# Performance work log

Hardware: AMD Instinct MI355X
Metric: run time of the kernel (lower is better)

The kernel has to match this reference:

```python
import jax, jax.numpy as jnp
import numpy as np

EPS = 1e-6  # clamp epsilon in GeM
NORM_EPS = 1e-12  # torch F.normalize eps
PATCH_SIZES = (3,)


def l2norm(x, axis):
    n = jnp.sqrt(jnp.sum(x * x, axis=axis, keepdims=True))
    return x / jnp.maximum(n, NORM_EPS)


def setup_inputs() -> dict:
    key = jax.random.key(0)
    k1, k2, k3 = jax.random.split(key, 3)
    N, D, H, W, F = 16, 2048, 32, 32, 512
    x = jax.random.normal(k1, (N, D, H, W), jnp.float32)
    proj_w = jax.random.normal(k2, (F, D), jnp.float32) * (1.0 / np.sqrt(D))
    proj_b = jax.random.normal(k3, (F,), jnp.float32) * 0.01
    p = jnp.full((1,), 3.0, jnp.float32)
    return {"x": x, "proj_w": proj_w, "proj_b": proj_b, "p": p}


def reference(x, proj_w, proj_b, p):
    # ---- GeM global descriptor (global_pool path inside local_pool) ----
    x = l2norm(x, axis=1)                                  # L2 over channel dim
    g = jnp.clip(x, EPS, None) ** p[0]                     # [N,D,H,W]
    g = g.mean(axis=(-2, -1))                              # [N,D]
    g = g ** (1.0 / p[0])
    g = g @ proj_w.T + proj_b                              # [N,F]
    g = l2norm(g, axis=1)

    # ---- integral image over spatial dims ----
    integ = jnp.cumsum(jnp.cumsum(x, axis=-1), axis=-2)    # [N,D,H,W]

    local_descs = []
    for ps in PATCH_SIZES:
        off = ps // 2
        # zero-pad (1+off) on top/left, then replicate-pad off on bottom/right
        ipad = jnp.pad(integ, ((0, 0), (0, 0), (1 + off, 0), (1 + off, 0)))
        ipad = jnp.pad(ipad, ((0, 0), (0, 0), (0, off), (0, off)), mode='edge')
        # box sum via 4-corner integral-image difference
        # == grouped 2x2 conv with dilation=ps, weights [[1,-1],[-1,1]], stride=1
        box = (ipad[:, :, :-ps, :-ps] - ipad[:, :, :-ps, ps:]
               - ipad[:, :, ps:, :-ps] + ipad[:, :, ps:, ps:])  # [N,D,H,W]
        N, D, Hh, Ww = box.shape
        pd = box.reshape(N, D, Hh * Ww).transpose(0, 2, 1)  # [N,HW,D]
        pd = pd @ proj_w.T + proj_b                         # [N,HW,F]
        pd = l2norm(pd, axis=2)
        local_descs.append(pd.transpose(0, 2, 1))           # [N,F,HW]

    return g, local_descs[0]
```

## Files before the change

### kernel.cpp

```cpp
#include <hip/hip_runtime.h>
#include <hip/hip_bf16.h>

#define N_ 16
#define D_ 2048
#define H_ 32
#define W_ 32
#define HW_ 1024
#define F_ 512

typedef unsigned short u16;
typedef unsigned int u32;
typedef __attribute__((ext_vector_type(8))) short bf16x8;
typedef __attribute__((ext_vector_type(4))) float f32x4;

__device__ __forceinline__ u16 f2bf(float f) {
  union { float fv; u32 u; } c; c.fv = f;
  u32 u = c.u;
  u32 r = (u + 0x7fffu + ((u >> 16) & 1u)) >> 16;
  return (u16)r;
}

#define GLD_LDS16(gp, lp) __builtin_amdgcn_global_load_lds( \
    (const __attribute__((address_space(1))) void*)(gp), \
    (__attribute__((address_space(3))) void*)(lp), 16, 0, 0)

__global__ __launch_bounds__(256) void k_zero(float* __restrict__ p) {
  int i = blockIdx.x * 256 + threadIdx.x;
  ((float4*)p)[i] = (float4){0.f, 0.f, 0.f, 0.f};
}

__global__ __launch_bounds__(256) void k_sumsq(const float* __restrict__ x, float* __restrict__ sumsq) {
  const int n = blockIdx.x;
  const int dc = blockIdx.y;
  const int t = threadIdx.x;
  const float* xp = x + ((size_t)n * D_ + (size_t)dc * 64) * HW_;
  float s0 = 0.f, s1 = 0.f, s2 = 0.f, s3 = 0.f;
  for (int d = 0; d < 64; ++d) {
    const float* row = xp + (size_t)d * HW_;
    float v0 = row[t], v1 = row[t + 256], v2 = row[t + 512], v3 = row[t + 768];
    s0 += v0 * v0; s1 += v1 * v1; s2 += v2 * v2; s3 += v3 * v3;
  }
  atomicAdd(&sumsq[n * HW_ + t      ], s0);
  atomicAdd(&sumsq[n * HW_ + t + 256], s1);
  atomicAdd(&sumsq[n * HW_ + t + 512], s2);
  atomicAdd(&sumsq[n * HW_ + t + 768], s3);
}

__global__ __launch_bounds__(256) void k_box2(const float* __restrict__ x,
    const float* __restrict__ sumsq, const float* __restrict__ pvec,
    float* __restrict__ gbuf, u16* __restrict__ packA) {
  const int n = blockIdx.x, ht = blockIdx.y, dc = blockIdx.z;
  const int h0 = ht * 4, d0 = dc * 64;
  const int t = threadIdx.x;
  const int w = t & 31, g = t >> 5;
  const float p = pvec[0];
  const bool p3 = (p == 3.0f);

  __shared__ __align__(16) u16 sbox[128 * 68];

  float rn[6];
  #pragma unroll
  for (int jj = 0; jj < 6; ++jj) {
    int hp = h0 - 1 + jj;
    float r = 0.f;
    if (hp >= 0 && hp < H_) r = 1.0f / fmaxf(sqrtf(sumsq[n * HW_ + hp * W_ + w]), 1e-12f);
    rn[jj] = r;
  }

  float s[8];
  #pragma unroll
  for (int j = 0; j < 8; ++j) s[j] = 0.f;

  #pragma unroll 2
  for (int j = 0; j < 8; ++j) {
    const int d = d0 + g * 8 + j;
    const float* col = x + ((size_t)(n * D_ + d)) * HW_ + w;
    float v[6];
    #pragma unroll
    for (int jj = 0; jj < 6; ++jj) {
      int hp = h0 - 1 + jj;
      float xv = (hp >= 0 && hp < H_) ? col[hp * W_] : 0.f;
      v[jj] = xv * rn[jj];
    }
    #pragma unroll
    for (int jj = 1; jj <= 4; ++jj) {
      float cv = fmaxf(v[jj], 1e-6f);
      s[j] += p3 ? cv * cv * cv : __powf(cv, p);
    }
    float hs[6];
    #pragma unroll
    for (int jj = 0; jj < 6; ++jj) {
      float l = __shfl_up(v[jj], 1, 32);
      float r = __shfl_down(v[jj], 1, 32);
      if (w == 0) l = 0.f;
      if (w == 31) r = 0.f;
      hs[jj] = l + v[jj] + r;
    }
    #pragma unroll
    for (int k = 0; k < 4; ++k) {
      float b = hs[k] + hs[k + 1] + hs[k + 2];
      sbox[(k * 32 + w) * 68 + g * 8 + j] = f2bf(b);
    }
  }
  __syncthreads();

  {
    const int r = t >> 1, half = t & 1;
    const u16* srcp = sbox + r * 68 + half * 32;
    uint2 a[8];
    #pragma unroll
    for (int q = 0; q < 8; ++q) a[q] = *(const uint2*)(srcp + q * 4);
    const int mt = n * 16 + ht * 2 + (r >> 6);
    const int mf = (r >> 4) & 3, r15 = r & 15;
    const int kt = dc * 2 + half;
    u16* dst = packA + ((size_t)(mt * 64 + kt) * 4 + mf) * 512 + r15 * 8;
    #pragma unroll
    for (int q = 0; q < 4; ++q) {
      uint4 b;
      b.x = a[2 * q].x; b.y = a[2 * q].y; b.z = a[2 * q + 1].x; b.w = a[2 * q + 1].y;
      *(uint4*)(dst + q * 128) = b;
    }
  }

  #pragma unroll
  for (int j = 0; j < 8; ++j) {
    float v = s[j];
    v += __shfl_xor(v, 16, 32);
    v += __shfl_xor(v, 8, 32);
    v += __shfl_xor(v, 4, 32);
    v += __shfl_xor(v, 2, 32);
    v += __shfl_xor(v, 1, 32);
    if (w == 0) atomicAdd(&gbuf[n * D_ + d0 + g * 8 + j], v);
  }
}

__global__ __launch_bounds__(256) void k_wconv(const float* __restrict__ w, u16* __restrict__ packB) {
  const int i = blockIdx.x * 256 + threadIdx.x;
  const int lane = i & 63, nf = (i >> 6) & 3, kt = (i >> 8) & 63, wq = i >> 14;
  const int r15 = lane & 15, hi = lane >> 4;
  const int f = wq * 64 + nf * 16 + r15;
  const int k = kt * 32 + hi * 8;
  const float* src = w + (size_t)f * D_ + k;
  float4 v0 = *(const float4*)(src);
  float4 v1 = *(const float4*)(src + 4);
  u16 r[8] = { f2bf(v0.x), f2bf(v0.y), f2bf(v0.z), f2bf(v0.w),
               f2bf(v1.x), f2bf(v1.y), f2bf(v1.z), f2bf(v1.w) };
  *(uint4*)(packB + (size_t)i * 8) = *(const uint4*)r;
}

__global__ __launch_bounds__(512) void k_gemm(const u16* __restrict__ packA,
    const u16* __restrict__ packB, const float* __restrict__ bias,
    float* __restrict__ outL) {
  const int n  = blockIdx.x >> 4;
  const int mtl = blockIdx.x & 15;
  const int mt = blockIdx.x;
  const int hw0 = mtl * 64;
  const int t = threadIdx.x;
  const int lane = t & 63, wv = t >> 6;
  const int r15 = lane & 15, hi = lane >> 4;

  __shared__ __align__(16) float smem_f[128 * 68];
  __shared__ float s_sq[8][64];
  __shared__ float s_rn[64];

  f32x4 acc[4][4];
  #pragma unroll
  for (int a = 0; a < 4; ++a)
    #pragma unroll
    for (int b = 0; b < 4; ++b) acc[a][b] = (f32x4){0.f, 0.f, 0.f, 0.f};

  const u16* asrc = packA + ((size_t)(mt * 64) * 4 + (wv & 3)) * 512 + lane * 8;
  const u16* bbase = packB + (size_t)wv * 131072 + lane * 8;

#define STAGE_A(KT) GLD_LDS16(asrc + (size_t)(KT) * 2048, \
    (char*)smem_f + ((KT) & 3) * 4096 + (wv & 3) * 1024)

  STAGE_A(0);
  STAGE_A(1);
  bf16x8 bc[4], bn[4];
  #pragma unroll
  for (int nf = 0; nf < 4; ++nf) bc[nf] = *(const bf16x8*)(bbase + nf * 512);

  for (int kt = 0; kt < 64; ++kt) {
    if (kt + 2 < 64) STAGE_A(kt + 2);
    if (kt + 1 < 64) {
      #pragma unroll
      for (int nf = 0; nf < 4; ++nf)
        bn[nf] = *(const bf16x8*)(bbase + ((kt + 1) * 4 + nf) * 512);
    }
    __builtin_amdgcn_sched_barrier(0);
    if (kt < 62) {
      asm volatile("s_waitcnt vmcnt(5)" ::: "memory");
    } else if (kt == 62) {
      asm volatile("s_waitcnt vmcnt(4)" ::: "memory");
    } else {
      asm volatile("s_waitcnt vmcnt(0)" ::: "memory");
    }
    __builtin_amdgcn_sched_barrier(0);
    __builtin_amdgcn_s_barrier();
    __builtin_amdgcn_sched_barrier(0);

    const u16* sA = (const u16*)((const char*)smem_f + (kt & 3) * 4096);
    bf16x8 af[4];
    #pragma unroll
    for (int mf = 0; mf < 4; ++mf)
      af[mf] = *(const bf16x8*)(sA + mf * 512 + lane * 8);
    #pragma unroll
    for (int mf = 0; mf < 4; ++mf)
      #pragma unroll
      for (int nf = 0; nf < 4; ++nf)
        acc[mf][nf] = __builtin_amdgcn_mfma_f32_16x16x32_bf16(af[mf], bc[nf], acc[mf][nf], 0, 0, 0);
    #pragma unroll
    for (int nf = 0; nf < 4; ++nf) bc[nf] = bn[nf];
  }
#undef STAGE_A

  float badd[4];
  #pragma unroll
  for (int nf = 0; nf < 4; ++nf) badd[nf] = bias[wv * 64 + nf * 16 + r15];
  #pragma unroll
  for (int mf = 0; mf < 4; ++mf)
    #pragma unroll
    for (int nf = 0; nf < 4; ++nf)
      #pragma unroll
      for (int j = 0; j < 4; ++j) acc[mf][nf][j] += badd[nf];

  #pragma unroll
  for (int mf = 0; mf < 4; ++mf)
    #pragma unroll
    for (int j = 0; j < 4; ++j) {
      float s = 0.f;
      #pragma unroll
      for (int nf = 0; nf < 4; ++nf) { float v = acc[mf][nf][j]; s += v * v; }
      s += __shfl_xor(s, 1); s += __shfl_xor(s, 2); s += __shfl_xor(s, 4); s += __shfl_xor(s, 8);
      if ((lane & 15) == 0) s_sq[wv][mf * 16 + hi * 4 + j] = s;
    }
  __syncthreads();
  if (t < 64) {
    float s = 0.f;
    #pragma unroll
    for (int w8 = 0; w8 < 8; ++w8) s += s_sq[w8][t];
    s_rn[t] = 1.0f / fmaxf(sqrtf(s), 1e-12f);
  }
  __syncthreads();

  float* ct = smem_f;
  for (int nf = 0; nf < 4; ++nf) {
    const int fi = wv * 16 + r15;
    #pragma unroll
    for (int mf = 0; mf < 4; ++mf)
      #pragma unroll
      for (int j = 0; j < 4; ++j) {
        int m = mf * 16 + hi * 4 + j;
        ct[fi * 68 + m] = acc[mf][nf][j] * s_rn[m];
      }
    __syncthreads();
    {
      int fr = t >> 2, mq = t & 3;
      int f = (fr >> 4) * 64 + nf * 16 + (fr & 15);
      float* dst = outL + ((size_t)(n * F_ + f)) * HW_ + hw0 + mq * 16;
      const float* srcp = ct + fr * 68 + mq * 16;
      float4 a0 = *(const float4*)(srcp);
      float4 a1 = *(const float4*)(srcp + 4);
      float4 a2 = *(const float4*)(srcp + 8);
      float4 a3 = *(const float4*)(srcp + 12);
      *(float4*)(dst) = a0; *(float4*)(dst + 4) = a1;
      *(float4*)(dst + 8) = a2; *(float4*)(dst + 12) = a3;
    }
    __syncthreads();
  }
}

__global__ __launch_bounds__(256) void k_gem_fin(const float* __restrict__ gbuf,
    const float* __restrict__ pvec, float* __restrict__ gg) {
  int i = blockIdx.x * 256 + threadIdx.x;
  float p = pvec[0];
  float m = gbuf[i] * (1.0f / 1024.0f);
  gg[i] = (p == 3.0f) ? cbrtf(m) : powf(m, 1.0f / p);
}

__global__ __launch_bounds__(256) void k_gproj(const float* __restrict__ w,
    const float* __restrict__ bias, const float* __restrict__ gg,
    float* __restrict__ gproj) {
  const int f = blockIdx.x;
  const int t = threadIdx.x;
  float wreg[8];
  #pragma unroll
  for (int j = 0; j < 8; ++j) wreg[j] = w[(size_t)f * D_ + t + j * 256];
  __shared__ float red[4];
  const int lane = t & 63, wv = t >> 6;
  for (int n = 0; n < N_; ++n) {
    float s = 0.f;
    #pragma unroll
    for (int j = 0; j < 8; ++j) s += wreg[j] * gg[n * D_ + t + j * 256];
    #pragma unroll
    for (int off = 32; off >= 1; off >>= 1) s += __shfl_down(s, off);
    if (lane == 0) red[wv] = s;
    __syncthreads();
    if (t == 0) gproj[n * F_ + f] = red[0] + red[1] + red[2] + red[3] + bias[f];
    __syncthreads();
  }
}

__global__ __launch_bounds__(512) void k_gnorm(const float* __restrict__ gproj, float* __restrict__ outg) {
  const int n = blockIdx.x;
  const int t = threadIdx.x;
  float v = gproj[n * F_ + t];
  float s = v * v;
  const int lane = t & 63, wv = t >> 6;
  #pragma unroll
  for (int off = 32; off >= 1; off >>= 1) s += __shfl_down(s, off);
  __shared__ float red[8];
  __shared__ float rtot;
  if (lane == 0) red[wv] = s;
  __syncthreads();
  if (t == 0) {
    float a = 0.f;
    #pragma unroll
    for (int i = 0; i < 8; ++i) a += red[i];
    rtot = 1.0f / fmaxf(sqrtf(a), 1e-12f);
  }
  __syncthreads();
  outg[n * F_ + t] = v * rtot;
}

extern "C" void kernel_launch(void* const* d_in, const int* in_sizes, int n_in,
                              void* d_out, int out_size, void* d_ws, size_t ws_size,
                              hipStream_t stream) {
  const float* x  = (const float*)d_in[0];
  const float* pw = (const float*)d_in[1];
  const float* pb = (const float*)d_in[2];
  const float* pv = (const float*)d_in[3];
  float* out = (float*)d_out;

  char* ws = (char*)d_ws;
  float* sumsq = (float*)ws;
  float* gbuf  = (float*)(ws + 65536);
  float* gg    = (float*)(ws + 65536 + 131072);
  float* gproj = (float*)(ws + 65536 + 2 * 131072);
  u16*   packB = (u16*)(ws + 65536 + 2 * 131072 + 32768);
  u16*   packA = (u16*)(ws + 4u * 1024u * 1024u);

  k_zero<<<dim3(48), dim3(256), 0, stream>>>(sumsq);
  k_sumsq<<<dim3(16, 32), dim3(256), 0, stream>>>(x, sumsq);
  k_wconv<<<dim3(512), dim3(256), 0, stream>>>(pw, packB);
  k_box2<<<dim3(16, 8, 32), dim3(256), 0, stream>>>(x, sumsq, pv, gbuf, packA);
  k_gem_fin<<<dim3(128), dim3(256), 0, stream>>>(gbuf, pv, gg);
  k_gproj<<<dim3(512), dim3(256), 0, stream>>>(pw, pb, gg, gproj);
  k_gnorm<<<dim3(16), dim3(512), 0, stream>>>(gproj, out);
  k_gemm<<<dim3(256), dim3(512), 0, stream>>>(packA, packB, pb, out + N_ * F_);
}
```

Measured before the change: 151.4 us.

## Fuse box-filter/GeM computation into the projection GEMM kernel

Removes the separate box kernel and the packed bf16 A buffer. The GEMM kernel now loads x directly per k-tile, normalizes, computes the 3x3 box sums through shared memory, accumulates GeM partial sums, and feeds bf16 fragments straight into MFMA. This saves the packA write and read round trip and one launch. In exchange each k-step gains two block barriers and serial box math in front of the MFMAs, and only 256 blocks do the box work, with 4-row halos overlapping between blocks.

```diff
diff --git a/kernel.cpp b/kernel.cpp
--- a/kernel.cpp
+++ b/kernel.cpp
@@ -14,15 +14,10 @@
 typedef __attribute__((ext_vector_type(4))) float f32x4;
 
 __device__ __forceinline__ u16 f2bf(float f) {
-  union { float fv; u32 u; } c; c.fv = f;
-  u32 u = c.u;
-  u32 r = (u + 0x7fffu + ((u >> 16) & 1u)) >> 16;
-  return (u16)r;
-}
-
-#define GLD_LDS16(gp, lp) __builtin_amdgcn_global_load_lds( \
-    (const __attribute__((address_space(1))) void*)(gp), \
-    (__attribute__((address_space(3))) void*)(lp), 16, 0, 0)
+  __hip_bfloat16 h = __float2bfloat16(f);
+  union { __hip_bfloat16 h; u16 u; } c; c.h = h;
+  return c.u;
+}
 
 __global__ __launch_bounds__(256) void k_zero(float* __restrict__ p) {
   int i = blockIdx.x * 256 + threadIdx.x;
@@ -44,94 +39,6 @@
   atomicAdd(&sumsq[n * HW_ + t + 256], s1);
   atomicAdd(&sumsq[n * HW_ + t + 512], s2);
   atomicAdd(&sumsq[n * HW_ + t + 768], s3);
-}
-
-__global__ __launch_bounds__(256) void k_box2(const float* __restrict__ x,
-    const float* __restrict__ sumsq, const float* __restrict__ pvec,
-    float* __restrict__ gbuf, u16* __restrict__ packA) {
-  const int n = blockIdx.x, ht = blockIdx.y, dc = blockIdx.z;
-  const int h0 = ht * 4, d0 = dc * 64;
-  const int t = threadIdx.x;
-  const int w = t & 31, g = t >> 5;
-  const float p = pvec[0];
-  const bool p3 = (p == 3.0f);
-
-  __shared__ __align__(16) u16 sbox[128 * 68];
-
-  float rn[6];
-  #pragma unroll
-  for (int jj = 0; jj < 6; ++jj) {
-    int hp = h0 - 1 + jj;
-    float r = 0.f;
-    if (hp >= 0 && hp < H_) r = 1.0f / fmaxf(sqrtf(sumsq[n * HW_ + hp * W_ + w]), 1e-12f);
-    rn[jj] = r;
-  }
-
-  float s[8];
-  #pragma unroll
-  for (int j = 0; j < 8; ++j) s[j] = 0.f;
-
-  #pragma unroll 2
-  for (int j = 0; j < 8; ++j) {
-    const int d = d0 + g * 8 + j;
-    const float* col = x + ((size_t)(n * D_ + d)) * HW_ + w;
-    float v[6];
-    #pragma unroll
-    for (int jj = 0; jj < 6; ++jj) {
-      int hp = h0 - 1 + jj;
-      float xv = (hp >= 0 && hp < H_) ? col[hp * W_] : 0.f;
-      v[jj] = xv * rn[jj];
-    }
-    #pragma unroll
-    for (int jj = 1; jj <= 4; ++jj) {
-      float cv = fmaxf(v[jj], 1e-6f);
-      s[j] += p3 ? cv * cv * cv : __powf(cv, p);
-    }
-    float hs[6];
-    #pragma unroll
-    for (int jj = 0; jj < 6; ++jj) {
-      float l = __shfl_up(v[jj], 1, 32);
-      float r = __shfl_down(v[jj], 1, 32);
-      if (w == 0) l = 0.f;
-      if (w == 31) r = 0.f;
-      hs[jj] = l + v[jj] + r;
-    }
-    #pragma unroll
-    for (int k = 0; k < 4; ++k) {
-      float b = hs[k] + hs[k + 1] + hs[k + 2];
-      sbox[(k * 32 + w) * 68 + g * 8 + j] = f2bf(b);
-    }
-  }
-  __syncthreads();
-
-  {
-    const int r = t >> 1, half = t & 1;
-    const u16* srcp = sbox + r * 68 + half * 32;
-    uint2 a[8];
-    #pragma unroll
-    for (int q = 0; q < 8; ++q) a[q] = *(const uint2*)(srcp + q * 4);
-    const int mt = n * 16 + ht * 2 + (r >> 6);
-    const int mf = (r >> 4) & 3, r15 = r & 15;
-    const int kt = dc * 2 + half;
-    u16* dst = packA + ((size_t)(mt * 64 + kt) * 4 + mf) * 512 + r15 * 8;
-    #pragma unroll
-    for (int q = 0; q < 4; ++q) {
-      uint4 b;
-      b.x = a[2 * q].x; b.y = a[2 * q].y; b.z = a[2 * q + 1].x; b.w = a[2 * q + 1].y;
-      *(uint4*)(dst + q * 128) = b;
-    }
-  }
-
-  #pragma unroll
-  for (int j = 0; j < 8; ++j) {
-    float v = s[j];
-    v += __shfl_xor(v, 16, 32);
-    v += __shfl_xor(v, 8, 32);
-    v += __shfl_xor(v, 4, 32);
-    v += __shfl_xor(v, 2, 32);
-    v += __shfl_xor(v, 1, 32);
-    if (w == 0) atomicAdd(&gbuf[n * D_ + d0 + g * 8 + j], v);
-  }
 }
 
 __global__ __launch_bounds__(256) void k_wconv(const float* __restrict__ w, u16* __restrict__ packB) {
@@ -148,73 +55,143 @@
   *(uint4*)(packB + (size_t)i * 8) = *(const uint4*)r;
 }
 
-__global__ __launch_bounds__(512) void k_gemm(const u16* __restrict__ packA,
+__global__ __launch_bounds__(512) void k_boxgemm(const float* __restrict__ x,
+    const float* __restrict__ sumsq, const float* __restrict__ pvec,
     const u16* __restrict__ packB, const float* __restrict__ bias,
-    float* __restrict__ outL) {
-  const int n  = blockIdx.x >> 4;
-  const int mtl = blockIdx.x & 15;
+    float* __restrict__ gbuf, float* __restrict__ outL) {
   const int mt = blockIdx.x;
-  const int hw0 = mtl * 64;
+  const int n  = mt >> 4;
+  const int hA = (mt & 15) * 2;
+  const int hw0 = (mt & 15) * 64;
   const int t = threadIdx.x;
   const int lane = t & 63, wv = t >> 6;
   const int r15 = lane & 15, hi = lane >> 4;
-
-  __shared__ __align__(16) float smem_f[128 * 68];
+  const int hp2 = t >> 8;
+  const int dd = (t & 255) >> 3;
+  const int w4 = t & 7, wq = w4 * 4;
+  const float p = pvec[0];
+  const bool p3c = (p == 3.0f);
+
+  __shared__ __align__(16) float smem[128 * 68];
+  float* hs = smem;
+  u16*   Af = (u16*)(smem + 4608);
+  float* rnl = smem + 4608 + 1024;
   __shared__ float s_sq[8][64];
   __shared__ float s_rn[64];
 
+  if (t < 128) {
+    int jj = t >> 5, w = t & 31;
+    int hp = hA - 1 + jj;
+    float r = 0.f;
+    if (hp >= 0 && hp < H_) r = 1.0f / fmaxf(sqrtf(sumsq[n * HW_ + hp * W_ + w]), 1e-12f);
+    rnl[jj * 32 + w] = r;
+  }
+  __syncthreads();
+
   f32x4 acc[4][4];
   #pragma unroll
   for (int a = 0; a < 4; ++a)
     #pragma unroll
     for (int b = 0; b < 4; ++b) acc[a][b] = (f32x4){0.f, 0.f, 0.f, 0.f};
 
-  const u16* asrc = packA + ((size_t)(mt * 64) * 4 + (wv & 3)) * 512 + lane * 8;
+  const int hpa0 = hA - 1 + hp2;
+  const int hpa1 = hA + 1 + hp2;
+  const bool val0 = (hpa0 >= 0);
+  const bool val1 = (hpa1 < H_);
+  const float* xb0 = x + ((size_t)(n * D_ + dd) * HW_ + (val0 ? hpa0 : 0) * W_ + wq);
+  const float* xb1 = x + ((size_t)(n * D_ + dd) * HW_ + (val1 ? hpa1 : 0) * W_ + wq);
+  const int hsoff0 = hp2 * 1152 + dd * 36 + wq;
+  const int hsoff1 = (hp2 + 2) * 1152 + dd * 36 + wq;
+  const float4 zero4 = {0.f, 0.f, 0.f, 0.f};
+
   const u16* bbase = packB + (size_t)wv * 131072 + lane * 8;
 
-#define STAGE_A(KT) GLD_LDS16(asrc + (size_t)(KT) * 2048, \
-    (char*)smem_f + ((KT) & 3) * 4096 + (wv & 3) * 1024)
-
-  STAGE_A(0);
-  STAGE_A(1);
+  float4 xa0 = val0 ? *(const float4*)(xb0) : zero4;
+  float4 xa1 = val1 ? *(const float4*)(xb1) : zero4;
   bf16x8 bc[4], bn[4];
   #pragma unroll
   for (int nf = 0; nf < 4; ++nf) bc[nf] = *(const bf16x8*)(bbase + nf * 512);
 
   for (int kt = 0; kt < 64; ++kt) {
-    if (kt + 2 < 64) STAGE_A(kt + 2);
-    if (kt + 1 < 64) {
+    float4 xn0, xn1;
+    if (kt < 63) {
+      const size_t xoff = (size_t)(kt + 1) * 32 * HW_;
+      xn0 = val0 ? *(const float4*)(xb0 + xoff) : zero4;
+      xn1 = val1 ? *(const float4*)(xb1 + xoff) : zero4;
       #pragma unroll
       for (int nf = 0; nf < 4; ++nf)
-        bn[nf] = *(const bf16x8*)(bbase + ((kt + 1) * 4 + nf) * 512);
-    }
-    __builtin_amdgcn_sched_barrier(0);
-    if (kt < 62) {
-      asm volatile("s_waitcnt vmcnt(5)" ::: "memory");
-    } else if (kt == 62) {
-      asm volatile("s_waitcnt vmcnt(4)" ::: "memory");
-    } else {
-      asm volatile("s_waitcnt vmcnt(0)" ::: "memory");
-    }
-    __builtin_amdgcn_sched_barrier(0);
-    __builtin_amdgcn_s_barrier();
-    __builtin_amdgcn_sched_barrier(0);
-
-    const u16* sA = (const u16*)((const char*)smem_f + (kt & 3) * 4096);
+        bn[nf] = *(const bf16x8*)(bbase + ((size_t)(kt + 1) * 4 + nf) * 512);
+    }
+
+    float4 rr0 = *(const float4*)(rnl + hp2 * 32 + wq);
+    float4 rr1 = *(const float4*)(rnl + (hp2 + 2) * 32 + wq);
+    float4 v0, v1;
+    v0.x = xa0.x * rr0.x; v0.y = xa0.y * rr0.y; v0.z = xa0.z * rr0.z; v0.w = xa0.w * rr0.w;
+    v1.x = xa1.x * rr1.x; v1.y = xa1.y * rr1.y; v1.z = xa1.z * rr1.z; v1.w = xa1.w * rr1.w;
+    {
+      float4 pk = hp2 ? v0 : v1;
+      float cx = fmaxf(pk.x, 1e-6f), cy = fmaxf(pk.y, 1e-6f);
+      float cz = fmaxf(pk.z, 1e-6f), cw = fmaxf(pk.w, 1e-6f);
+      float g;
+      if (p3c) g = cx * cx * cx + cy * cy * cy + cz * cz * cz + cw * cw * cw;
+      else     g = __powf(cx, p) + __powf(cy, p) + __powf(cz, p) + __powf(cw, p);
+      g += __shfl_xor(g, 1, 8);
+      g += __shfl_xor(g, 2, 8);
+      g += __shfl_xor(g, 4, 8);
+      if (w4 == 0) atomicAdd(&gbuf[n * D_ + kt * 32 + dd], g);
+    }
+    {
+      float lf = __shfl_up(v0.w, 1, 8), rf = __shfl_down(v0.x, 1, 8);
+      if (w4 == 0) lf = 0.f;
+      if (w4 == 7) rf = 0.f;
+      float4 h;
+      h.x = lf + v0.x + v0.y;  h.y = v0.x + v0.y + v0.z;
+      h.z = v0.y + v0.z + v0.w; h.w = v0.z + v0.w + rf;
+      *(float4*)(hs + hsoff0) = h;
+    }
+    {
+      float lf = __shfl_up(v1.w, 1, 8), rf = __shfl_down(v1.x, 1, 8);
+      if (w4 == 0) lf = 0.f;
+      if (w4 == 7) rf = 0.f;
+      float4 h;
+      h.x = lf + v1.x + v1.y;  h.y = v1.x + v1.y + v1.z;
+      h.z = v1.y + v1.z + v1.w; h.w = v1.z + v1.w + rf;
+      *(float4*)(hs + hsoff1) = h;
+    }
+    __syncthreads();
+
+    {
+      const float* hb = hs + hp2 * 1152 + dd * 36 + wq;
+      float4 h0 = *(const float4*)(hb);
+      float4 h1 = *(const float4*)(hb + 1152);
+      float4 h2 = *(const float4*)(hb + 2304);
+      float o[4] = { h0.x + h1.x + h2.x, h0.y + h1.y + h2.y,
+                     h0.z + h1.z + h2.z, h0.w + h1.w + h2.w };
+      const int hii = dd >> 3, jj = dd & 7;
+      #pragma unroll
+      for (int i = 0; i < 4; ++i) {
+        int r = hp2 * 32 + wq + i;
+        Af[(r >> 4) * 512 + hii * 128 + (r & 15) * 8 + jj] = f2bf(o[i]);
+      }
+    }
+    __syncthreads();
+
     bf16x8 af[4];
     #pragma unroll
     for (int mf = 0; mf < 4; ++mf)
-      af[mf] = *(const bf16x8*)(sA + mf * 512 + lane * 8);
+      af[mf] = *(const bf16x8*)(Af + mf * 512 + lane * 8);
     #pragma unroll
     for (int mf = 0; mf < 4; ++mf)
       #pragma unroll
       for (int nf = 0; nf < 4; ++nf)
         acc[mf][nf] = __builtin_amdgcn_mfma_f32_16x16x32_bf16(af[mf], bc[nf], acc[mf][nf], 0, 0, 0);
+
+    xa0 = xn0; xa1 = xn1;
     #pragma unroll
     for (int nf = 0; nf < 4; ++nf) bc[nf] = bn[nf];
   }
-#undef STAGE_A
-
+
+  __syncthreads();
   float badd[4];
   #pragma unroll
   for (int nf = 0; nf < 4; ++nf) badd[nf] = bias[wv * 64 + nf * 16 + r15];
@@ -244,7 +221,7 @@
   }
   __syncthreads();
 
-  float* ct = smem_f;
+  float* ct = smem;
   for (int nf = 0; nf < 4; ++nf) {
     const int fi = wv * 16 + r15;
     #pragma unroll
@@ -339,14 +316,12 @@
   float* gg    = (float*)(ws + 65536 + 131072);
   float* gproj = (float*)(ws + 65536 + 2 * 131072);
   u16*   packB = (u16*)(ws + 65536 + 2 * 131072 + 32768);
-  u16*   packA = (u16*)(ws + 4u * 1024u * 1024u);
 
   k_zero<<<dim3(48), dim3(256), 0, stream>>>(sumsq);
   k_sumsq<<<dim3(16, 32), dim3(256), 0, stream>>>(x, sumsq);
   k_wconv<<<dim3(512), dim3(256), 0, stream>>>(pw, packB);
-  k_box2<<<dim3(16, 8, 32), dim3(256), 0, stream>>>(x, sumsq, pv, gbuf, packA);
+  k_boxgemm<<<dim3(256), dim3(512), 0, stream>>>(x, sumsq, pv, packB, pb, gbuf, out + N_ * F_);
   k_gem_fin<<<dim3(128), dim3(256), 0, stream>>>(gbuf, pv, gg);
   k_gproj<<<dim3(512), dim3(256), 0, stream>>>(pw, pb, gg, gproj);
   k_gnorm<<<dim3(16), dim3(512), 0, stream>>>(gproj, out);
-  k_gemm<<<dim3(256), dim3(512), 0, stream>>>(packA, packB, pb, out + N_ * F_);
-}
+}
```

After: 141.0 us. 6.8% less time.

## Apply box filter after projection to read x once and shrink box work

Applied to the files above, without the earlier changes.

The input x is now read in a single pass: each block converts raw x to bf16, packs it for the GEMM and accumulates the per-pixel sum of squares, so the separate sumsq pass over x is gone. Because the box sum and the per-pixel L2 scale are linear, the GEMM runs on raw x, applies the pixel normalization in its epilogue, and a new kernel performs the 3x3 box sum, adds bias and does the per-descriptor L2 norm on the F=512 projected output instead of D=2048 channels. GeM statistics are computed by a separate pass over the packed bf16 data, so they now use bf16-rounded values, and the projected tensor makes an extra round trip through global memory.

```diff
diff --git a/kernel.cpp b/kernel.cpp
--- a/kernel.cpp
+++ b/kernel.cpp
@@ -14,11 +14,16 @@
 typedef __attribute__((ext_vector_type(4))) float f32x4;
 
 __device__ __forceinline__ u16 f2bf(float f) {
-  union { float fv; u32 u; } c; c.fv = f;
-  u32 u = c.u;
-  u32 r = (u + 0x7fffu + ((u >> 16) & 1u)) >> 16;
-  return (u16)r;
-}
+  __hip_bfloat16 h = __float2bfloat16(f);
+  union { __hip_bfloat16 h; u16 u; } c; c.h = h;
+  return c.u;
+}
+__device__ __forceinline__ u32 f2bf2(float lo, float hi) {
+  return (u32)f2bf(lo) | ((u32)f2bf(hi) << 16);
+}
+__device__ __forceinline__ float bflo(u32 u) { union { u32 u; float f; } c; c.u = u << 16; return c.f; }
+__device__ __forceinline__ float bfhi(u32 u) { union { u32 u; float f; } c; c.u = u & 0xffff0000u; return c.f; }
+__device__ __forceinline__ float bfu(u16 u) { union { u32 u; float f; } c; c.u = (u32)u << 16; return c.f; }
 
 #define GLD_LDS16(gp, lp) __builtin_amdgcn_global_load_lds( \
     (const __attribute__((address_space(1))) void*)(gp), \
@@ -29,87 +34,48 @@
   ((float4*)p)[i] = (float4){0.f, 0.f, 0.f, 0.f};
 }
 
-__global__ __launch_bounds__(256) void k_sumsq(const float* __restrict__ x, float* __restrict__ sumsq) {
-  const int n = blockIdx.x;
-  const int dc = blockIdx.y;
-  const int t = threadIdx.x;
-  const float* xp = x + ((size_t)n * D_ + (size_t)dc * 64) * HW_;
-  float s0 = 0.f, s1 = 0.f, s2 = 0.f, s3 = 0.f;
-  for (int d = 0; d < 64; ++d) {
-    const float* row = xp + (size_t)d * HW_;
-    float v0 = row[t], v1 = row[t + 256], v2 = row[t + 512], v3 = row[t + 768];
-    s0 += v0 * v0; s1 += v1 * v1; s2 += v2 * v2; s3 += v3 * v3;
-  }
-  atomicAdd(&sumsq[n * HW_ + t      ], s0);
-  atomicAdd(&sumsq[n * HW_ + t + 256], s1);
-  atomicAdd(&sumsq[n * HW_ + t + 512], s2);
-  atomicAdd(&sumsq[n * HW_ + t + 768], s3);
-}
-
-__global__ __launch_bounds__(256) void k_box2(const float* __restrict__ x,
-    const float* __restrict__ sumsq, const float* __restrict__ pvec,
-    float* __restrict__ gbuf, u16* __restrict__ packA) {
+__global__ __launch_bounds__(256) void k_sumsqpack(const float* __restrict__ x,
+    float* __restrict__ sumsq, u16* __restrict__ packA) {
   const int n = blockIdx.x, ht = blockIdx.y, dc = blockIdx.z;
   const int h0 = ht * 4, d0 = dc * 64;
   const int t = threadIdx.x;
-  const int w = t & 31, g = t >> 5;
-  const float p = pvec[0];
-  const bool p3 = (p == 3.0f);
-
-  __shared__ __align__(16) u16 sbox[128 * 68];
-
-  float rn[6];
-  #pragma unroll
-  for (int jj = 0; jj < 6; ++jj) {
-    int hp = h0 - 1 + jj;
-    float r = 0.f;
-    if (hp >= 0 && hp < H_) r = 1.0f / fmaxf(sqrtf(sumsq[n * HW_ + hp * W_ + w]), 1e-12f);
-    rn[jj] = r;
-  }
-
-  float s[8];
-  #pragma unroll
-  for (int j = 0; j < 8; ++j) s[j] = 0.f;
-
-  #pragma unroll 2
-  for (int j = 0; j < 8; ++j) {
-    const int d = d0 + g * 8 + j;
-    const float* col = x + ((size_t)(n * D_ + d)) * HW_ + w;
-    float v[6];
-    #pragma unroll
-    for (int jj = 0; jj < 6; ++jj) {
-      int hp = h0 - 1 + jj;
-      float xv = (hp >= 0 && hp < H_) ? col[hp * W_] : 0.f;
-      v[jj] = xv * rn[jj];
-    }
-    #pragma unroll
-    for (int jj = 1; jj <= 4; ++jj) {
-      float cv = fmaxf(v[jj], 1e-6f);
-      s[j] += p3 ? cv * cv * cv : __powf(cv, p);
-    }
-    float hs[6];
-    #pragma unroll
-    for (int jj = 0; jj < 6; ++jj) {
-      float l = __shfl_up(v[jj], 1, 32);
-      float r = __shfl_down(v[jj], 1, 32);
-      if (w == 0) l = 0.f;
-      if (w == 31) r = 0.f;
-      hs[jj] = l + v[jj] + r;
-    }
-    #pragma unroll
-    for (int k = 0; k < 4; ++k) {
-      float b = hs[k] + hs[k + 1] + hs[k + 2];
-      sbox[(k * 32 + w) * 68 + g * 8 + j] = f2bf(b);
-    }
+  const int w4 = t & 7, dg = t >> 3, wq = w4 * 4;
+
+  __shared__ __align__(16) u32 sbox[128 * 34];
+
+  const float* base0 = x + ((size_t)(n * D_ + d0 + dg * 2)) * HW_ + wq;
+  const float* base1 = base0 + HW_;
+
+  #pragma unroll
+  for (int jj = 0; jj < 4; ++jj) {
+    const int hp = h0 + jj;
+    float4 a = *(const float4*)(base0 + hp * W_);
+    float4 b = *(const float4*)(base1 + hp * W_);
+    const int rb = jj * 32 + wq;
+    sbox[(rb + 0) * 34 + dg] = f2bf2(a.x, b.x);
+    sbox[(rb + 1) * 34 + dg] = f2bf2(a.y, b.y);
+    sbox[(rb + 2) * 34 + dg] = f2bf2(a.z, b.z);
+    sbox[(rb + 3) * 34 + dg] = f2bf2(a.w, b.w);
   }
   __syncthreads();
 
   {
     const int r = t >> 1, half = t & 1;
-    const u16* srcp = sbox + r * 68 + half * 32;
+    const u32* srcp = sbox + r * 34 + half * 16;
     uint2 a[8];
     #pragma unroll
-    for (int q = 0; q < 8; ++q) a[q] = *(const uint2*)(srcp + q * 4);
+    for (int q = 0; q < 8; ++q) a[q] = *(const uint2*)(srcp + q * 2);
+
+    float s = 0.f;
+    #pragma unroll
+    for (int q = 0; q < 8; ++q) {
+      float v0 = bflo(a[q].x), v1 = bfhi(a[q].x);
+      float v2 = bflo(a[q].y), v3 = bfhi(a[q].y);
+      s += v0 * v0 + v1 * v1 + v2 * v2 + v3 * v3;
+    }
+    s += __shfl_xor(s, 1);
+    if (half == 0) atomicAdd(&sumsq[n * HW_ + ht * 128 + r], s);
+
     const int mt = n * 16 + ht * 2 + (r >> 6);
     const int mf = (r >> 4) & 3, r15 = r & 15;
     const int kt = dc * 2 + half;
@@ -121,16 +87,53 @@
       *(uint4*)(dst + q * 128) = b;
     }
   }
-
-  #pragma unroll
-  for (int j = 0; j < 8; ++j) {
-    float v = s[j];
-    v += __shfl_xor(v, 16, 32);
-    v += __shfl_xor(v, 8, 32);
-    v += __shfl_xor(v, 4, 32);
-    v += __shfl_xor(v, 2, 32);
-    v += __shfl_xor(v, 1, 32);
-    if (w == 0) atomicAdd(&gbuf[n * D_ + d0 + g * 8 + j], v);
+}
+
+__global__ __launch_bounds__(256) void k_gempass(const u16* __restrict__ packA,
+    const float* __restrict__ sumsq, const float* __restrict__ pvec,
+    float* __restrict__ gbuf) {
+  const int n = blockIdx.x, kt = blockIdx.y;
+  const int t = threadIdx.x, lane = t & 63, wv = t >> 6;
+  const int r15 = lane & 15, hi = lane >> 4;
+  const float p = pvec[0];
+  const bool p3 = (p == 3.0f);
+
+  __shared__ float rnl[1024];
+  __shared__ float gtmp[4][32];
+
+  for (int i = t; i < 1024; i += 256)
+    rnl[i] = 1.0f / fmaxf(sqrtf(sumsq[n * HW_ + i]), 1e-12f);
+  __syncthreads();
+
+  float accv[8];
+  #pragma unroll
+  for (int e = 0; e < 8; ++e) accv[e] = 0.f;
+
+  for (int mt = 0; mt < 16; ++mt) {
+    const u16* src = packA + ((size_t)((n * 16 + mt) * 64 + kt) * 4 + wv) * 512 + lane * 8;
+    bf16x8 v = *(const bf16x8*)src;
+    float rnv = rnl[mt * 64 + wv * 16 + r15];
+    #pragma unroll
+    for (int e = 0; e < 8; ++e) {
+      float c = fmaxf(bfu((u16)v[e]) * rnv, 1e-6f);
+      accv[e] += p3 ? c * c * c : __powf(c, p);
+    }
+  }
+  #pragma unroll
+  for (int e = 0; e < 8; ++e) {
+    accv[e] += __shfl_xor(accv[e], 1, 16);
+    accv[e] += __shfl_xor(accv[e], 2, 16);
+    accv[e] += __shfl_xor(accv[e], 4, 16);
+    accv[e] += __shfl_xor(accv[e], 8, 16);
+  }
+  if (r15 == 0) {
+    #pragma unroll
+    for (int e = 0; e < 8; ++e) gtmp[wv][hi * 8 + e] = accv[e];
+  }
+  __syncthreads();
+  if (t < 32) {
+    float g = gtmp[0][t] + gtmp[1][t] + gtmp[2][t] + gtmp[3][t];
+    gbuf[n * D_ + kt * 32 + t] = g;
   }
 }
 
@@ -143,14 +146,14 @@
   const float* src = w + (size_t)f * D_ + k;
   float4 v0 = *(const float4*)(src);
   float4 v1 = *(const float4*)(src + 4);
-  u16 r[8] = { f2bf(v0.x), f2bf(v0.y), f2bf(v0.z), f2bf(v0.w),
-               f2bf(v1.x), f2bf(v1.y), f2bf(v1.z), f2bf(v1.w) };
+  u32 r[4] = { f2bf2(v0.x, v0.y), f2bf2(v0.z, v0.w),
+               f2bf2(v1.x, v1.y), f2bf2(v1.z, v1.w) };
   *(uint4*)(packB + (size_t)i * 8) = *(const uint4*)r;
 }
 
 __global__ __launch_bounds__(512) void k_gemm(const u16* __restrict__ packA,
-    const u16* __restrict__ packB, const float* __restrict__ bias,
-    float* __restrict__ outL) {
+    const u16* __restrict__ packB, const float* __restrict__ sumsq,
+    float* __restrict__ y) {
   const int n  = blockIdx.x >> 4;
   const int mtl = blockIdx.x & 15;
   const int mt = blockIdx.x;
@@ -160,7 +163,6 @@
   const int r15 = lane & 15, hi = lane >> 4;
 
   __shared__ __align__(16) float smem_f[128 * 68];
-  __shared__ float s_sq[8][64];
   __shared__ float s_rn[64];
 
   f32x4 acc[4][4];
@@ -215,33 +217,8 @@
   }
 #undef STAGE_A
 
-  float badd[4];
-  #pragma unroll
-  for (int nf = 0; nf < 4; ++nf) badd[nf] = bias[wv * 64 + nf * 16 + r15];
-  #pragma unroll
-  for (int mf = 0; mf < 4; ++mf)
-    #pragma unroll
-    for (int nf = 0; nf < 4; ++nf)
-      #pragma unroll
-      for (int j = 0; j < 4; ++j) acc[mf][nf][j] += badd[nf];
-
-  #pragma unroll
-  for (int mf = 0; mf < 4; ++mf)
-    #pragma unroll
-    for (int j = 0; j < 4; ++j) {
-      float s = 0.f;
-      #pragma unroll
-      for (int nf = 0; nf < 4; ++nf) { float v = acc[mf][nf][j]; s += v * v; }
-      s += __shfl_xor(s, 1); s += __shfl_xor(s, 2); s += __shfl_xor(s, 4); s += __shfl_xor(s, 8);
-      if ((lane & 15) == 0) s_sq[wv][mf * 16 + hi * 4 + j] = s;
-    }
-  __syncthreads();
-  if (t < 64) {
-    float s = 0.f;
-    #pragma unroll
-    for (int w8 = 0; w8 < 8; ++w8) s += s_sq[w8][t];
-    s_rn[t] = 1.0f / fmaxf(sqrtf(s), 1e-12f);
-  }
+  __syncthreads();
+  if (t < 64) s_rn[t] = 1.0f / fmaxf(sqrtf(sumsq[n * HW_ + hw0 + t]), 1e-12f);
   __syncthreads();
 
   float* ct = smem_f;
@@ -258,7 +235,7 @@
     {
       int fr = t >> 2, mq = t & 3;
       int f = (fr >> 4) * 64 + nf * 16 + (fr & 15);
-      float* dst = outL + ((size_t)(n * F_ + f)) * HW_ + hw0 + mq * 16;
+      float* dst = y + ((size_t)(n * F_ + f)) * HW_ + hw0 + mq * 16;
       const float* srcp = ct + fr * 68 + mq * 16;
       float4 a0 = *(const float4*)(srcp);
       float4 a1 = *(const float4*)(srcp + 4);
@@ -268,6 +245,53 @@
       *(float4*)(dst + 8) = a2; *(float4*)(dst + 12) = a3;
     }
     __syncthreads();
+  }
+}
+
+__global__ __launch_bounds__(512) void k_boxf(const float* __restrict__ y,
+    const float* __restrict__ bias, float* __restrict__ pdt,
+    float* __restrict__ outL) {
+  const int n = blockIdx.x, hb = blockIdx.y;
+  const int t = threadIdx.x, lane = t & 63, wv = t >> 6;
+  const int h1 = lane >> 5, w = lane & 31;
+  const int h_out = hb * 2 + h1;
+
+  __shared__ float wsq[8][64];
+  __shared__ float srn[64];
+
+  const size_t ybase = (size_t)n * F_ * HW_;
+  float* pbase = pdt + ((size_t)(n * 16 + hb)) * F_ * 64;
+
+  float accsq = 0.f;
+  const bool up_ok = (h_out - 1 >= 0), dn_ok = (h_out + 1 < H_);
+  for (int it = 0; it < 64; ++it) {
+    const int f = wv * 64 + it;
+    const float* yf = y + ybase + (size_t)f * HW_;
+    float l0 = up_ok ? yf[(h_out - 1) * W_ + w] : 0.f;
+    float l1 = yf[h_out * W_ + w];
+    float l2 = dn_ok ? yf[(h_out + 1) * W_ + w] : 0.f;
+    float vs = l0 + l1 + l2;
+    float lf = __shfl_up(vs, 1, 32);
+    float rf = __shfl_down(vs, 1, 32);
+    if (w == 0) lf = 0.f;
+    if (w == 31) rf = 0.f;
+    float pd = lf + vs + rf + bias[f];
+    accsq += pd * pd;
+    pbase[(size_t)f * 64 + lane] = pd;
+  }
+  wsq[wv][lane] = accsq;
+  __syncthreads();
+  if (t < 64) {
+    float s = 0.f;
+    #pragma unroll
+    for (int w8 = 0; w8 < 8; ++w8) s += wsq[w8][t];
+    srn[t] = 1.0f / fmaxf(sqrtf(s), 1e-12f);
+  }
+  __syncthreads();
+  for (int it = 0; it < 64; ++it) {
+    const int f = wv * 64 + it;
+    float pv = pbase[(size_t)f * 64 + lane];
+    outL[ybase + (size_t)f * HW_ + hb * 64 + lane] = pv * srn[lane];
   }
 }
 
@@ -340,13 +364,16 @@
   float* gproj = (float*)(ws + 65536 + 2 * 131072);
   u16*   packB = (u16*)(ws + 65536 + 2 * 131072 + 32768);
   u16*   packA = (u16*)(ws + 4u * 1024u * 1024u);
-
-  k_zero<<<dim3(48), dim3(256), 0, stream>>>(sumsq);
-  k_sumsq<<<dim3(16, 32), dim3(256), 0, stream>>>(x, sumsq);
+  float* ybuf  = (float*)(ws + 68u * 1024u * 1024u);
+  float* pdt   = (float*)(ws + 100u * 1024u * 1024u);
+
+  k_zero<<<dim3(16), dim3(256), 0, stream>>>(sumsq);
   k_wconv<<<dim3(512), dim3(256), 0, stream>>>(pw, packB);
-  k_box2<<<dim3(16, 8, 32), dim3(256), 0, stream>>>(x, sumsq, pv, gbuf, packA);
+  k_sumsqpack<<<dim3(16, 8, 32), dim3(256), 0, stream>>>(x, sumsq, packA);
+  k_gempass<<<dim3(16, 64), dim3(256), 0, stream>>>(packA, sumsq, pv, gbuf);
   k_gem_fin<<<dim3(128), dim3(256), 0, stream>>>(gbuf, pv, gg);
   k_gproj<<<dim3(512), dim3(256), 0, stream>>>(pw, pb, gg, gproj);
   k_gnorm<<<dim3(16), dim3(512), 0, stream>>>(gproj, out);
-  k_gemm<<<dim3(256), dim3(512), 0, stream>>>(packA, packB, pb, out + N_ * F_);
-}
+  k_gemm<<<dim3(256), dim3(512), 0, stream>>>(packA, packB, sumsq, ybuf);
+  k_boxf<<<dim3(16, 16), dim3(512), 0, stream>>>(ybuf, pb, pdt, out + N_ * F_);
+}
```

New measurement: 163.7 us. +8.1%, slower.
